# Kernel optimization log

Measured on AMD Instinct MI355X. Metric: run time of the kernel, lower is better.

The kernel has to match this reference:

```python
import jax, jax.numpy as jnp
import numpy as np

ENTITIES_N = 100000
RELATIONS_N = 1000
Z_SIZE = 128
BATCH = 1024


def setup_inputs() -> dict:
    key = jax.random.key(0)
    kz, kh, kr, kt = jax.random.split(key, 4)
    return {
        "z": jax.random.normal(kz, (BATCH, Z_SIZE), dtype=jnp.float32),
        "hID": jax.random.randint(kh, (BATCH,), 0, ENTITIES_N, dtype=jnp.int64) if jax.config.jax_enable_x64 else jax.random.randint(kh, (BATCH,), 0, ENTITIES_N, dtype=jnp.int32),
        "rID": jax.random.randint(kr, (BATCH,), 0, RELATIONS_N, dtype=jnp.int32),
        "tID": jax.random.randint(kt, (BATCH,), 0, ENTITIES_N, dtype=jnp.int32),
    }


def reference(z, hID, rID, tID):
    # Original forward ignores the Linear+Tanh model and z's values entirely;
    # it builds, per row, one_hot(h, E) ++ one_hot(r, R) ++ one_hot(t, E) as float.
    B = z.shape[0]
    width = ENTITIES_N + RELATIONS_N + ENTITIES_N  # 2E + R
    rows = jnp.arange(B)
    # Column offsets for the three one-hot segments; single fused scatter.
    cols = jnp.stack(
        [hID.astype(jnp.int32),
         ENTITIES_N + rID.astype(jnp.int32),
         ENTITIES_N + RELATIONS_N + tID.astype(jnp.int32)],
        axis=1)  # [B, 3]
    out = jnp.zeros((B, width), dtype=jnp.float32)
    out = out.at[rows[:, None], cols].set(1.0)
    return out
```

## Files before the change

### kernel.cpp

```cpp
#include <hip/hip_runtime.h>

#define ENTITIES_N 100000
#define RELATIONS_N 1000
#define WIDTH (2 * ENTITIES_N + RELATIONS_N)
#define BATCH_MAX 1024

__global__ void scatter_ones_i32(const int* __restrict__ hID,
                                 const int* __restrict__ rID,
                                 const int* __restrict__ tID,
                                 float* __restrict__ out, int batch) {
    int row = blockIdx.x * blockDim.x + threadIdx.x;
    if (row >= batch) return;
    long long base = (long long)row * WIDTH;
    out[base + (long long)hID[row]] = 1.0f;
    out[base + ENTITIES_N + (long long)rID[row]] = 1.0f;
    out[base + ENTITIES_N + RELATIONS_N + (long long)tID[row]] = 1.0f;
}

__global__ void scatter_ones_i64(const long long* __restrict__ hID,
                                 const int* __restrict__ rID,
                                 const int* __restrict__ tID,
                                 float* __restrict__ out, int batch) {
    int row = blockIdx.x * blockDim.x + threadIdx.x;
    if (row >= batch) return;
    long long base = (long long)row * WIDTH;
    out[base + hID[row]] = 1.0f;
    out[base + ENTITIES_N + (long long)rID[row]] = 1.0f;
    out[base + ENTITIES_N + RELATIONS_N + (long long)tID[row]] = 1.0f;
}

extern "C" void kernel_launch(void* const* d_in, const int* in_sizes, int n_in,
                              void* d_out, int out_size, void* d_ws, size_t ws_size,
                              hipStream_t stream) {
    const int* rID = (const int*)d_in[2];
    const int* tID = (const int*)d_in[3];
    float* out = (float*)d_out;

    const int batch = in_sizes[2];

    hipMemsetAsync(d_out, 0, (size_t)out_size * sizeof(float), stream);

    const int block = 256;
    const int grid = (batch + block - 1) / block;
    if (in_sizes[1] == batch) {
        scatter_ones_i32<<<grid, block, 0, stream>>>((const int*)d_in[1], rID, tID, out, batch);
    } else {
        scatter_ones_i64<<<grid, block, 0, stream>>>((const long long*)d_in[1], rID, tID, out, batch);
    }
}
```

Before: 777.4 us.

## Fuse zero-fill and one-hot scatter into single vectorized row-writing kernel

Replaces the memset followed by a tiny scatter kernel with one 2D-grid kernel in which each thread computes and writes four output floats, setting each to 1 where its column matches h, r or t. Stores are float4 and nontemporal. This removes the separate memset pass and its launch, and aims for full-bandwidth streaming writes. It drops the int64 hID path and assumes WIDTH is divisible by 4.

After: 820.1 us. +5.5%, slower.

```diff
diff --git a/kernel.cpp b/kernel.cpp
--- a/kernel.cpp
+++ b/kernel.cpp
@@ -3,48 +3,44 @@
 #define ENTITIES_N 100000
 #define RELATIONS_N 1000
 #define WIDTH (2 * ENTITIES_N + RELATIONS_N)
-#define BATCH_MAX 1024
+#define QWIDTH (WIDTH / 4)
 
-__global__ void scatter_ones_i32(const int* __restrict__ hID,
-                                 const int* __restrict__ rID,
-                                 const int* __restrict__ tID,
-                                 float* __restrict__ out, int batch) {
-    int row = blockIdx.x * blockDim.x + threadIdx.x;
-    if (row >= batch) return;
-    long long base = (long long)row * WIDTH;
-    out[base + (long long)hID[row]] = 1.0f;
-    out[base + ENTITIES_N + (long long)rID[row]] = 1.0f;
-    out[base + ENTITIES_N + RELATIONS_N + (long long)tID[row]] = 1.0f;
-}
+typedef float vfloat4 __attribute__((ext_vector_type(4)));
 
-__global__ void scatter_ones_i64(const long long* __restrict__ hID,
-                                 const int* __restrict__ rID,
-                                 const int* __restrict__ tID,
-                                 float* __restrict__ out, int batch) {
-    int row = blockIdx.x * blockDim.x + threadIdx.x;
-    if (row >= batch) return;
-    long long base = (long long)row * WIDTH;
-    out[base + hID[row]] = 1.0f;
-    out[base + ENTITIES_N + (long long)rID[row]] = 1.0f;
-    out[base + ENTITIES_N + RELATIONS_N + (long long)tID[row]] = 1.0f;
+__global__ __launch_bounds__(256) void onehot_rows(
+        const int* __restrict__ hID,
+        const int* __restrict__ rID,
+        const int* __restrict__ tID,
+        vfloat4* __restrict__ out) {
+    const int q = blockIdx.x * blockDim.x + threadIdx.x;
+    if (q >= QWIDTH) return;
+    const int row = blockIdx.y;
+    const int col = q * 4;
+
+    const int h = hID[row];
+    const int r = ENTITIES_N + rID[row];
+    const int t = ENTITIES_N + RELATIONS_N + tID[row];
+
+    vfloat4 v;
+    v.x = (col     == h || col     == r || col     == t) ? 1.0f : 0.0f;
+    v.y = (col + 1 == h || col + 1 == r || col + 1 == t) ? 1.0f : 0.0f;
+    v.z = (col + 2 == h || col + 2 == r || col + 2 == t) ? 1.0f : 0.0f;
+    v.w = (col + 3 == h || col + 3 == r || col + 3 == t) ? 1.0f : 0.0f;
+
+    __builtin_nontemporal_store(v, &out[(long long)row * QWIDTH + q]);
 }
 
 extern "C" void kernel_launch(void* const* d_in, const int* in_sizes, int n_in,
                               void* d_out, int out_size, void* d_ws, size_t ws_size,
                               hipStream_t stream) {
+    const int* hID = (const int*)d_in[1];
     const int* rID = (const int*)d_in[2];
     const int* tID = (const int*)d_in[3];
-    float* out = (float*)d_out;
+    vfloat4* out = (vfloat4*)d_out;
 
     const int batch = in_sizes[2];
 
-    hipMemsetAsync(d_out, 0, (size_t)out_size * sizeof(float), stream);
-
     const int block = 256;
-    const int grid = (batch + block - 1) / block;
-    if (in_sizes[1] == batch) {
-        scatter_ones_i32<<<grid, block, 0, stream>>>((const int*)d_in[1], rID, tID, out, batch);
-    } else {
-        scatter_ones_i64<<<grid, block, 0, stream>>>((const long long*)d_in[1], rID, tID, out, batch);
-    }
+    dim3 grid((QWIDTH + block - 1) / block, batch);
+    onehot_rows<<<grid, block, 0, stream>>>(hID, rID, tID, out);
 }
```
